# Kernel optimization log

Measured on AMD Instinct MI355X. Metric: run time of the kernel, lower is better.

## Reference

```python
import jax, jax.numpy as jnp
import numpy as np

B, S, T = 16, 256, 256
E, H = 1024, 512          # embedded_size = 2*hidden_size (required by the module's math)
ENV, ZHV = 32000, 32000


def gru_layer(x, h0, Wih, Whh, bih, bhh):
    # x: [B,T,in], h0: [B,H]; PyTorch GRU cell semantics
    xp = jnp.einsum('bti,gi->btg', x, Wih) + bih  # precompute input projections [B,T,3H]

    def step(h, xp_t):
        hp = h @ Whh.T + bhh
        xr, xz, xn = jnp.split(xp_t, 3, axis=-1)
        hr, hz, hn = jnp.split(hp, 3, axis=-1)
        r = jax.nn.sigmoid(xr + hr)
        z = jax.nn.sigmoid(xz + hz)
        n = jnp.tanh(xn + r * hn)
        h_new = (1.0 - z) * n + z * h
        return h_new, h_new

    h_last, ys = jax.lax.scan(step, h0, jnp.swapaxes(xp, 0, 1))
    return jnp.swapaxes(ys, 0, 1), h_last


def gru2(x, h0, p0, p1):
    # 2-layer stacked GRU; h0: [2,B,H]
    y0, h0f = gru_layer(x, h0[0], *p0)
    y1, h1f = gru_layer(y0, h0[1], *p1)
    return y1, jnp.stack([h0f, h1f])


def setup_inputs() -> dict:
    key = jax.random.key(0)
    ks = jax.random.split(key, 32)
    s = 0.05
    f = jnp.float32
    inp = {}
    inp['en_sen'] = jax.random.randint(ks[0], (B, S), 0, ENV)
    inp['zh_sen'] = jax.random.randint(ks[1], (B, T), 0, ZHV)
    inp['en_emb'] = (jax.random.normal(ks[2], (ENV, E)) * s).astype(f)
    inp['zh_emb'] = (jax.random.normal(ks[3], (ZHV, E)) * s).astype(f)
    inp['h0'] = jax.random.normal(ks[4], (2, B, H)).astype(f)
    i = 5
    for tag, in0 in (('e', E), ('d', E)):
        for layer, ind in ((0, in0), (1, H)):
            inp[f'Wih_{tag}{layer}'] = (jax.random.normal(ks[i], (3 * H, ind)) * s).astype(f); i += 1
            inp[f'Whh_{tag}{layer}'] = (jax.random.normal(ks[i], (3 * H, H)) * s).astype(f); i += 1
            inp[f'bih_{tag}{layer}'] = jnp.zeros((3 * H,), f)
            inp[f'bhh_{tag}{layer}'] = jnp.zeros((3 * H,), f)
    inp['fcW'] = (jax.random.normal(ks[i], (ZHV, E)) * s).astype(f)
    inp['fcb'] = jnp.zeros((ZHV,), f)
    return inp


def reference(en_sen, zh_sen, en_emb, zh_emb, h0,
              Wih_e0, Whh_e0, bih_e0, bhh_e0, Wih_e1, Whh_e1, bih_e1, bhh_e1,
              Wih_d0, Whh_d0, bih_d0, bhh_d0, Wih_d1, Whh_d1, bih_d1, bhh_d1,
              fcW, fcb):
    # encoder
    ex = en_emb[en_sen]                                     # [B,S,E]
    en_out, hid = gru2(ex, h0, (Wih_e0, Whh_e0, bih_e0, bhh_e0),
                       (Wih_e1, Whh_e1, bih_e1, bhh_e1))    # [B,S,H], [2,B,H]
    # shift target right with SOS token (zh_vocab_size - 2)
    sos = jnp.full((B, 1), ZHV - 2, dtype=zh_sen.dtype)
    zh = jnp.concatenate([sos, zh_sen[:, :-1]], axis=1)
    zx = zh_emb[zh]                                         # [B,T,E]
    # decoder (teacher forcing = 1.0 -> full-sequence scan is exact)
    dec_out, _ = gru2(zx, hid, (Wih_d0, Whh_d0, bih_d0, bhh_d0),
                      (Wih_d1, Whh_d1, bih_d1, bhh_d1))     # [B,T,H]
    # dot-product attention over encoder states, per decoder timestep
    scores = jnp.einsum('bsh,bth->bst', en_out, dec_out)    # [B,S,T]
    attn = jax.nn.softmax(scores, axis=1)                   # softmax over source dim
    ctx = jnp.einsum('bst,bsh->bth', attn, en_out)          # [B,T,H]
    de = jnp.concatenate([dec_out, ctx], axis=-1)           # [B,T,2H] == [B,T,E]
    out = de.reshape(-1, E) @ fcW.T + fcb                   # [B*T, ZHV]
    return out
```

## Files before the change

### kernel.cpp

```cpp
#include <hip/hip_runtime.h>
#include <math.h>

#define B_ 16
#define S_ 256
#define T_ 256
#define E_ 1024
#define H_ 512
#define G_ 1536
#define V_ 32000

typedef unsigned short u16;
typedef unsigned int u32;
typedef short short8 __attribute__((ext_vector_type(8)));
typedef short short4v __attribute__((ext_vector_type(4)));
typedef float f32x4 __attribute__((ext_vector_type(4)));

__device__ inline u16 f2bf(float x) {
  union { float f; unsigned u; } a; a.f = x;
  unsigned r = a.u + 0x7fff + ((a.u >> 16) & 1);
  return (u16)(r >> 16);
}
__device__ inline void split2(float x, u16& hi, u16& lo) {
  union { float f; unsigned u; } a; a.f = x;
  hi = (u16)(a.u >> 16);
  union { unsigned u; float f; } b; b.u = a.u & 0xffff0000u;
  lo = f2bf(x - b.f);
}

__device__ inline f32x4 load_f4_coh(const float* p) {
  f32x4 v;
  asm volatile("global_load_dwordx4 %0, %1, off sc0 sc1" : "=v"(v) : "v"(p));
  return v;
}

__device__ inline float dot4(f32x4 a, f32x4 b) {
  return a.x * b.x + a.y * b.y + a.z * b.z + a.w * b.w;
}

__global__ __launch_bounds__(256) void k_embed_enc(const int* __restrict__ sen,
                                                   const float* __restrict__ emb,
                                                   float* __restrict__ out) {
  long row = blockIdx.x;
  int tid = threadIdx.x;
  long e = sen[row];
  float4 v = *(const float4*)(emb + e * E_ + tid * 4);
  *(float4*)(out + row * E_ + tid * 4) = v;
}

__global__ __launch_bounds__(256) void k_embed_dec(const int* __restrict__ zh,
                                                   const float* __restrict__ emb,
                                                   float* __restrict__ out) {
  long row = blockIdx.x;
  int b = (int)(row >> 8), t = (int)(row & 255);
  int tid = threadIdx.x;
  long e = (t == 0) ? (V_ - 2) : zh[b * T_ + t - 1];
  float4 v = *(const float4*)(emb + e * E_ + tid * 4);
  *(float4*)(out + row * E_ + tid * 4) = v;
}

__global__ __launch_bounds__(256) void k_transpose(const float* __restrict__ in,
                                                   float* __restrict__ out, int R, int C) {
  __shared__ float tile[32][33];
  long z = blockIdx.z;
  const float* inz = in + z * (long)R * C;
  float* outz = out + z * (long)R * C;
  int x = blockIdx.x * 32 + threadIdx.x;
  int y0 = blockIdx.y * 32;
#pragma unroll
  for (int i = threadIdx.y; i < 32; i += 8)
    tile[i][threadIdx.x] = inz[(long)(y0 + i) * C + x];
  __syncthreads();
  int xo = y0 + threadIdx.x;
#pragma unroll
  for (int i = threadIdx.y; i < 32; i += 8) {
    int yo = blockIdx.x * 32 + i;
    outz[(long)yo * R + xo] = tile[threadIdx.x][i];
  }
}

__global__ __launch_bounds__(256) void k_gemm_nt(
    const float* __restrict__ A, int lda, const float* __restrict__ A2, int lda2, int kSplit,
    const float* __restrict__ Bm, int ldb, const float* __restrict__ bias,
    float* __restrict__ C, int ldc, int K, long sA, long sB, long sC) {
  __shared__ float As[8][132];
  __shared__ float Bs[8][132];
  int z = blockIdx.z;
  A += z * sA;
  Bm += z * sB;
  C += z * sC;
  int tid = threadIdx.x;
  int bm = blockIdx.y * 128, bn = blockIdx.x * 128;
  int tx = tid & 15, ty = tid >> 4;
  int lr = tid >> 1, lc = (tid & 1) * 4;
  float acc[8][8] = {};
  for (int k0 = 0; k0 < K; k0 += 8) {
    int ka = k0 + lc;
    const float* ap;
    if (A2 != nullptr && ka >= kSplit)
      ap = A2 + (long)(bm + lr) * lda2 + (ka - kSplit);
    else
      ap = A + (long)(bm + lr) * lda + ka;
    float4 a4 = *(const float4*)ap;
    float4 b4 = *(const float4*)(Bm + (long)(bn + lr) * ldb + k0 + lc);
    As[lc + 0][lr] = a4.x; As[lc + 1][lr] = a4.y; As[lc + 2][lr] = a4.z; As[lc + 3][lr] = a4.w;
    Bs[lc + 0][lr] = b4.x; Bs[lc + 1][lr] = b4.y; Bs[lc + 2][lr] = b4.z; Bs[lc + 3][lr] = b4.w;
    __syncthreads();
#pragma unroll
    for (int kk = 0; kk < 8; kk++) {
      float ar[8], br[8];
      *(float4*)&ar[0] = *(const float4*)&As[kk][ty * 8];
      *(float4*)&ar[4] = *(const float4*)&As[kk][ty * 8 + 4];
      *(float4*)&br[0] = *(const float4*)&Bs[kk][tx * 8];
      *(float4*)&br[4] = *(const float4*)&Bs[kk][tx * 8 + 4];
#pragma unroll
      for (int i = 0; i < 8; i++)
#pragma unroll
        for (int j = 0; j < 8; j++) acc[i][j] += ar[i] * br[j];
    }
    __syncthreads();
  }
  float bv[8];
#pragma unroll
  for (int j = 0; j < 8; j++) bv[j] = bias ? bias[bn + tx * 8 + j] : 0.f;
#pragma unroll
  for (int i = 0; i < 8; i++) {
    float* cp = C + (long)(bm + ty * 8 + i) * ldc + bn + tx * 8;
    float4 o0, o1;
    o0.x = acc[i][0] + bv[0]; o0.y = acc[i][1] + bv[1];
    o0.z = acc[i][2] + bv[2]; o0.w = acc[i][3] + bv[3];
    o1.x = acc[i][4] + bv[4]; o1.y = acc[i][5] + bv[5];
    o1.z = acc[i][6] + bv[6]; o1.w = acc[i][7] + bv[7];
    *(float4*)cp = o0;
    *(float4*)(cp + 4) = o1;
  }
}


__global__ __launch_bounds__(256) void k_gemm_mfma_nt(
    const float* __restrict__ A, int lda, const float* __restrict__ A2, int lda2, int kSplit,
    const float* __restrict__ Bm, int ldb, const float* __restrict__ bias,
    float* __restrict__ C, int ldc, int K) {
  __shared__ short8 Ah[512], Al[512], Bh[512], Bl[512];
  int tid = threadIdx.x;
  int bm = blockIdx.y * 128, bn = blockIdx.x * 128;
  int wave = tid >> 6, lane = tid & 63;
  int wm = (wave >> 1) * 64, wn = (wave & 1) * 64;
  int srow = tid >> 1, scol = (tid & 1) * 16, q0 = (tid & 1) * 2;
  int fr = lane & 15, fq = lane >> 4;
  int ubase = (srow >> 6) * 256 + ((srow >> 4) & 3) * 64;
  int ua0 = ubase + q0 * 16 + ((srow & 15) ^ (q0 * 2));
  int ua1 = ubase + (q0 + 1) * 16 + ((srow & 15) ^ (q0 * 2 + 2));
  int abase = (wm >> 6) * 256 + fq * 16 + (fr ^ (fq * 2));
  int bbase = (wn >> 6) * 256 + fq * 16 + (fr ^ (fq * 2));

  f32x4 acc[4][4] = {};

  for (int k0 = 0; k0 < K; k0 += 32) {
    {
      int ka = k0 + scol;
      const float* ap;
      if (A2 != nullptr && ka >= kSplit)
        ap = A2 + (long)(bm + srow) * lda2 + (ka - kSplit);
      else
        ap = A + (long)(bm + srow) * lda + ka;
      float va[16];
      *(float4*)&va[0] = *(const float4*)ap;
      *(float4*)&va[4] = *(const float4*)(ap + 4);
      *(float4*)&va[8] = *(const float4*)(ap + 8);
      *(float4*)&va[12] = *(const float4*)(ap + 12);
      u16 h[16], l[16];
#pragma unroll
      for (int i = 0; i < 16; i++) split2(va[i], h[i], l[i]);
      Ah[ua0] = *(short8*)&h[0];
      Ah[ua1] = *(short8*)&h[8];
      Al[ua0] = *(short8*)&l[0];
      Al[ua1] = *(short8*)&l[8];
    }
    {
      const float* bp = Bm + (long)(bn + srow) * ldb + k0 + scol;
      float vb[16];
      *(float4*)&vb[0] = *(const float4*)bp;
      *(float4*)&vb[4] = *(const float4*)(bp + 4);
      *(float4*)&vb[8] = *(const float4*)(bp + 8);
      *(float4*)&vb[12] = *(const float4*)(bp + 12);
      u16 h[16], l[16];
#pragma unroll
      for (int i = 0; i < 16; i++) split2(vb[i], h[i], l[i]);
      Bh[ua0] = *(short8*)&h[0];
      Bh[ua1] = *(short8*)&h[8];
      Bl[ua0] = *(short8*)&l[0];
      Bl[ua1] = *(short8*)&l[8];
    }
    __syncthreads();
    short8 afh[4], afl[4];
#pragma unroll
    for (int mt = 0; mt < 4; mt++) {
      afh[mt] = Ah[abase + mt * 64];
      afl[mt] = Al[abase + mt * 64];
    }
#pragma unroll
    for (int nt = 0; nt < 4; nt++) {
      short8 bh = Bh[bbase + nt * 64];
      short8 bl = Bl[bbase + nt * 64];
#pragma unroll
      for (int mt = 0; mt < 4; mt++) {
        acc[mt][nt] = __builtin_amdgcn_mfma_f32_16x16x32_bf16(afh[mt], bh, acc[mt][nt], 0, 0, 0);
        acc[mt][nt] = __builtin_amdgcn_mfma_f32_16x16x32_bf16(afh[mt], bl, acc[mt][nt], 0, 0, 0);
        acc[mt][nt] = __builtin_amdgcn_mfma_f32_16x16x32_bf16(afl[mt], bh, acc[mt][nt], 0, 0, 0);
      }
    }
    __syncthreads();
  }
  int fq4 = fq * 4;
#pragma unroll
  for (int nt = 0; nt < 4; nt++) {
    int col = bn + wn + nt * 16 + fr;
    float bv = bias ? bias[col] : 0.f;
#pragma unroll
    for (int mt = 0; mt < 4; mt++) {
      int row = bm + wm + mt * 16 + fq4;
#pragma unroll
      for (int j = 0; j < 4; j++)
        C[(long)(row + j) * ldc + col] = acc[mt][nt][j] + bv;
    }
  }
}

__global__ __launch_bounds__(256) void k_presplit(const float* __restrict__ src,
                                                  u16* __restrict__ hi,
                                                  u16* __restrict__ lo) {
  long i0 = ((long)blockIdx.x * 256 + threadIdx.x) * 8;
  float v[8];
  *(float4*)&v[0] = *(const float4*)(src + i0);
  *(float4*)&v[4] = *(const float4*)(src + i0 + 4);
  u16 h[8], l[8];
#pragma unroll
  for (int i = 0; i < 8; i++) split2(v[i], h[i], l[i]);
  *(short8*)(hi + i0) = *(short8*)&h[0];
  *(short8*)(lo + i0) = *(short8*)&l[0];
}

__global__ __launch_bounds__(256) void k_presplit_cat(const float* __restrict__ a,
                                                      const float* __restrict__ b,
                                                      u16* __restrict__ hi,
                                                      u16* __restrict__ lo) {
  long row = blockIdx.x;
  int tid = threadIdx.x;
  const float* src = (tid < 128) ? (a + row * 512 + tid * 4)
                                 : (b + row * 512 + (tid - 128) * 4);
  float4 v = *(const float4*)src;
  u16 h[4], l[4];
  split2(v.x, h[0], l[0]); split2(v.y, h[1], l[1]);
  split2(v.z, h[2], l[2]); split2(v.w, h[3], l[3]);
  *(short4v*)(hi + row * 1024 + tid * 4) = *(short4v*)&h[0];
  *(short4v*)(lo + row * 1024 + tid * 4) = *(short4v*)&l[0];
}

__global__ __launch_bounds__(256) void k_gemm_bf16p_nt(
    const u16* __restrict__ Ahi, const u16* __restrict__ Alo,
    const u16* __restrict__ Bhi, const u16* __restrict__ Blo,
    const float* __restrict__ bias, float* __restrict__ C, int ldc, int K) {
  __shared__ short8 Ah[512], Al[512], Bh[512], Bl[512];
  int tid = threadIdx.x;
  int bm = blockIdx.x * 128, bn = blockIdx.y * 128;
  int wave = tid >> 6, lane = tid & 63;
  int wm = (wave >> 1) * 64, wn = (wave & 1) * 64;
  int srow = tid >> 1, scol = (tid & 1) * 16, q0 = (tid & 1) * 2;
  int fr = lane & 15, fq = lane >> 4;
  int ubase = (srow >> 6) * 256 + ((srow >> 4) & 3) * 64;
  int ua0 = ubase + q0 * 16 + ((srow & 15) ^ (q0 * 2));
  int ua1 = ubase + (q0 + 1) * 16 + ((srow & 15) ^ (q0 * 2 + 2));
  int abase = (wm >> 6) * 256 + fq * 16 + (fr ^ (fq * 2));
  int bbase = (wn >> 6) * 256 + fq * 16 + (fr ^ (fq * 2));

  f32x4 acc[4][4] = {};
  long aoff = (long)(bm + srow) * K + scol;
  long boff = (long)(bn + srow) * K + scol;

  for (int k0 = 0; k0 < K; k0 += 32) {
    short8 ah0 = *(const short8*)(Ahi + aoff + k0);
    short8 ah1 = *(const short8*)(Ahi + aoff + k0 + 8);
    short8 al0 = *(const short8*)(Alo + aoff + k0);
    short8 al1 = *(const short8*)(Alo + aoff + k0 + 8);
    short8 bh0 = *(const short8*)(Bhi + boff + k0);
    short8 bh1 = *(const short8*)(Bhi + boff + k0 + 8);
    short8 bl0 = *(const short8*)(Blo + boff + k0);
    short8 bl1 = *(const short8*)(Blo + boff + k0 + 8);
    Ah[ua0] = ah0; Ah[ua1] = ah1;
    Al[ua0] = al0; Al[ua1] = al1;
    Bh[ua0] = bh0; Bh[ua1] = bh1;
    Bl[ua0] = bl0; Bl[ua1] = bl1;
    __syncthreads();
    short8 afh[4], afl[4];
#pragma unroll
    for (int mt = 0; mt < 4; mt++) {
      afh[mt] = Ah[abase + mt * 64];
      afl[mt] = Al[abase + mt * 64];
    }
#pragma unroll
    for (int nt = 0; nt < 4; nt++) {
      short8 bh = Bh[bbase + nt * 64];
      short8 bl = Bl[bbase + nt * 64];
#pragma unroll
      for (int mt = 0; mt < 4; mt++) {
        acc[mt][nt] = __builtin_amdgcn_mfma_f32_16x16x32_bf16(afh[mt], bh, acc[mt][nt], 0, 0, 0);
        acc[mt][nt] = __builtin_amdgcn_mfma_f32_16x16x32_bf16(afh[mt], bl, acc[mt][nt], 0, 0, 0);
        acc[mt][nt] = __builtin_amdgcn_mfma_f32_16x16x32_bf16(afl[mt], bh, acc[mt][nt], 0, 0, 0);
      }
    }
    __syncthreads();
  }
  int fq4 = fq * 4;
#pragma unroll
  for (int nt = 0; nt < 4; nt++) {
    int col = bn + wn + nt * 16 + fr;
    float bv = bias ? bias[col] : 0.f;
#pragma unroll
    for (int mt = 0; mt < 4; mt++) {
      int row = bm + wm + mt * 16 + fq4;
#pragma unroll
      for (int j = 0; j < 4; j++)
        C[(long)(row + j) * ldc + col] = acc[mt][nt][j] + bv;
    }
  }
}

#define WSLOT 32
__global__ __launch_bounds__(256) void k_gru_b(
    const float* __restrict__ xp, float* __restrict__ y,
    const float* __restrict__ Whh, const float* __restrict__ bhh,
    const float* __restrict__ hinit, long hbs, int* __restrict__ ep) {
  __shared__ float hls[536];
  int tid = threadIdx.x;
  int wave = tid >> 6, lane = tid & 63;
  int jsub = lane >> 5, ksl = lane & 31;
  int b = blockIdx.x >> 4, js = blockIdx.x & 15;
  int jbase = js * 32 + wave * 8 + jsub * 4;

  f32x4 w[4][3][4];
  float bb[4][3];
#pragma unroll
  for (int e = 0; e < 4; e++)
#pragma unroll
    for (int g = 0; g < 3; g++) {
      const float* r = Whh + (long)(g * 512 + jbase + e) * 512 + ksl * 16;
#pragma unroll
      for (int q = 0; q < 4; q++) w[e][g][q] = *(const f32x4*)(r + q * 4);
      bb[e][g] = bhh[g * 512 + jbase + e];
    }
  bool gl = (ksl < 4);
  int jme = jbase + ksl;
  const int* epb = ep + (long)(b * 16 + (lane & 15)) * WSLOT;
  int* epMine = ep + (long)(b * 16 + js) * WSLOT;
  float* yb = y + (long)b * (256 * 512);
  const float* xpb = xp + (long)b * (256 * 1536);

  for (int t = 0; t < 256; t++) {
    float xr = 0.f, xz = 0.f, xn = 0.f;
    if (gl) {
      const float* xpt = xpb + (long)t * 1536 + jme;
      xr = xpt[0]; xz = xpt[512]; xn = xpt[1024];
    }
    if (t > 0) {
      if (wave == 0) {
        while (true) {
          int e0;
          asm volatile("global_load_dword %0, %1, off sc0 sc1" : "=v"(e0) : "v"(epb));
          asm volatile("s_waitcnt vmcnt(0)" ::: "memory");
          if (__ballot(e0 >= t) == ~0ull) break;
          __builtin_amdgcn_s_sleep(1);
        }
      }
      __syncthreads();
    }
    if (tid < 128) {
      const float* src = (t == 0) ? (hinit + (long)b * hbs + tid * 4)
                                  : (yb + (long)(t - 1) * 512 + tid * 4);
      f32x4 v = load_f4_coh(src);
      asm volatile("s_waitcnt vmcnt(0)" ::: "memory");
      __builtin_amdgcn_sched_barrier(0);
      *(f32x4*)&hls[(tid & 3) * 132 + (tid >> 2) * 4] = v;
    }
    __syncthreads();
    f32x4 h0 = *(const f32x4*)&hls[ksl * 4];
    f32x4 h1 = *(const f32x4*)&hls[132 + ksl * 4];
    f32x4 h2 = *(const f32x4*)&hls[264 + ksl * 4];
    f32x4 h3 = *(const f32x4*)&hls[396 + ksl * 4];
    float a[4][3];
#pragma unroll
    for (int e = 0; e < 4; e++)
#pragma unroll
      for (int g = 0; g < 3; g++)
        a[e][g] = dot4(h0, w[e][g][0]) + dot4(h1, w[e][g][1]) +
                  dot4(h2, w[e][g][2]) + dot4(h3, w[e][g][3]);
#pragma unroll
    for (int m = 1; m <= 16; m <<= 1)
#pragma unroll
      for (int e = 0; e < 4; e++) {
        a[e][0] += __shfl_xor(a[e][0], m);
        a[e][1] += __shfl_xor(a[e][1], m);
        a[e][2] += __shfl_xor(a[e][2], m);
      }
    if (gl) {
      float hr = 0.f, hz = 0.f, hn = 0.f, Br = 0.f, Bz = 0.f, Bn = 0.f;
#pragma unroll
      for (int e = 0; e < 4; e++)
        if (ksl == e) {
          hr = a[e][0]; hz = a[e][1]; hn = a[e][2];
          Br = bb[e][0]; Bz = bb[e][1]; Bn = bb[e][2];
        }
      float r = 1.f / (1.f + __expf(-(xr + hr + Br)));
      float z = 1.f / (1.f + __expf(-(xz + hz + Bz)));
      float n = tanhf(xn + r * (hn + Bn));
      float hp = hls[((jme >> 2) & 3) * 132 + (jme >> 4) * 4 + (jme & 3)];
      float hv = (1.f - z) * n + z * hp;
      __hip_atomic_store(&yb[(long)t * 512 + jme], hv,
                         __ATOMIC_RELAXED, __HIP_MEMORY_SCOPE_AGENT);
    }
    asm volatile("s_waitcnt vmcnt(0)" ::: "memory");
    __syncthreads();
    if (tid == 0)
      __hip_atomic_store(epMine, t + 1, __ATOMIC_RELAXED, __HIP_MEMORY_SCOPE_AGENT);
  }
}

__global__ __launch_bounds__(256) void k_softmax(float* __restrict__ p) {
  long row = blockIdx.x;
  int tid = threadIdx.x;
  float* pr = p + row * 256;
  float v = pr[tid];
  float m = v;
#pragma unroll
  for (int off = 32; off >= 1; off >>= 1) m = fmaxf(m, __shfl_xor(m, off));
  __shared__ float wmax[4];
  __shared__ float wsum[4];
  int wv = tid >> 6, ln = tid & 63;
  if (ln == 0) wmax[wv] = m;
  __syncthreads();
  m = fmaxf(fmaxf(wmax[0], wmax[1]), fmaxf(wmax[2], wmax[3]));
  float e = expf(v - m);
  float s = e;
#pragma unroll
  for (int off = 32; off >= 1; off >>= 1) s += __shfl_xor(s, off);
  if (ln == 0) wsum[wv] = s;
  __syncthreads();
  s = wsum[0] + wsum[1] + wsum[2] + wsum[3];
  pr[tid] = e / s;
}

extern "C" void kernel_launch(void* const* d_in, const int* in_sizes, int n_in,
                              void* d_out, int out_size, void* d_ws, size_t ws_size,
                              hipStream_t stream) {
  const int* en_sen = (const int*)d_in[0];
  const int* zh_sen = (const int*)d_in[1];
  const float* en_emb = (const float*)d_in[2];
  const float* zh_emb = (const float*)d_in[3];
  const float* h0 = (const float*)d_in[4];
  const float* Wih_e0 = (const float*)d_in[5];
  const float* Whh_e0 = (const float*)d_in[6];
  const float* bih_e0 = (const float*)d_in[7];
  const float* bhh_e0 = (const float*)d_in[8];
  const float* Wih_e1 = (const float*)d_in[9];
  const float* Whh_e1 = (const float*)d_in[10];
  const float* bih_e1 = (const float*)d_in[11];
  const float* bhh_e1 = (const float*)d_in[12];
  const float* Wih_d0 = (const float*)d_in[13];
  const float* Whh_d0 = (const float*)d_in[14];
  const float* bih_d0 = (const float*)d_in[15];
  const float* bhh_d0 = (const float*)d_in[16];
  const float* Wih_d1 = (const float*)d_in[17];
  const float* Whh_d1 = (const float*)d_in[18];
  const float* bih_d1 = (const float*)d_in[19];
  const float* bhh_d1 = (const float*)d_in[20];
  const float* fcW = (const float*)d_in[21];
  const float* fcb = (const float*)d_in[22];
  float* out = (float*)d_out;

  const size_t needFast = (2ull * 32768000 + 2ull * 4194304) * sizeof(u16);
  bool fastFC = (ws_size >= needFast);

  u16* fcWhi = (u16*)d_ws;
  u16* fcWlo = fcWhi + 32768000;
  u16* Ahi = (u16*)(fcWlo + 32768000);
  u16* Alo = Ahi + 4194304;

  int* flags = (int*)d_out;
  float* bufE = (float*)d_out + 32768;
  float* xp = bufE + 4194304;
  float* bufY = xp + 6291456;
  float* enOut = bufY + 2097152;
  float* scT = enOut + 2097152;
  float* enOutT = scT + 1048576;
  float* decOutA = enOutT + 2097152;
  float* ctxA = decOutA + 2097152;

  float* decOut = fastFC ? decOutA : (float*)d_ws;
  float* ctx = fastFC ? ctxA : ((float*)d_ws + 2097152);

  hipMemsetAsync(flags, 0, 32768 * sizeof(int), stream);

  dim3 tb(32, 8);

  if (fastFC)
    k_presplit<<<16000, 256, 0, stream>>>(fcW, fcWhi, fcWlo);

  k_embed_enc<<<B_ * S_, 256, 0, stream>>>(en_sen, en_emb, bufE);
  k_gemm_mfma_nt<<<dim3(G_ / 128, (B_ * S_) / 128, 1), 256, 0, stream>>>(
      bufE, E_, nullptr, 0, E_, Wih_e0, E_, bih_e0, xp, G_, E_);
  k_gru_b<<<256, 256, 0, stream>>>(xp, bufY, Whh_e0, bhh_e0, h0, (long)H_, flags);
  k_gemm_mfma_nt<<<dim3(G_ / 128, (B_ * S_) / 128, 1), 256, 0, stream>>>(
      bufY, H_, nullptr, 0, H_, Wih_e1, H_, bih_e1, xp, G_, H_);
  k_gru_b<<<256, 256, 0, stream>>>(xp, enOut, Whh_e1, bhh_e1, h0 + B_ * H_, (long)H_,
                                   flags + 8192);

  k_embed_dec<<<B_ * T_, 256, 0, stream>>>(zh_sen, zh_emb, bufE);
  k_gemm_mfma_nt<<<dim3(G_ / 128, (B_ * T_) / 128, 1), 256, 0, stream>>>(
      bufE, E_, nullptr, 0, E_, Wih_d0, E_, bih_d0, xp, G_, E_);
  k_gru_b<<<256, 256, 0, stream>>>(xp, bufY, Whh_d0, bhh_d0, bufY + 255 * H_,
                                   (long)(256 * H_), flags + 16384);
  k_gemm_mfma_nt<<<dim3(G_ / 128, (B_ * T_) / 128, 1), 256, 0, stream>>>(
      bufY, H_, nullptr, 0, H_, Wih_d1, H_, bih_d1, xp, G_, H_);
  k_gru_b<<<256, 256, 0, stream>>>(xp, decOut, Whh_d1, bhh_d1, enOut + 255 * H_,
                                   (long)(256 * H_), flags + 24576);

  k_gemm_nt<<<dim3(S_ / 128, T_ / 128, B_), 256, 0, stream>>>(
      decOut, H_, nullptr, 0, H_, enOut, H_, nullptr, scT, S_, H_,
      (long)T_ * H_, (long)S_ * H_, (long)T_ * S_);
  k_softmax<<<B_ * T_, 256, 0, stream>>>(scT);
  k_transpose<<<dim3(16, 8, B_), tb, 0, stream>>>(enOut, enOutT, 256, 512);
  k_gemm_nt<<<dim3(H_ / 128, T_ / 128, B_), 256, 0, stream>>>(
      scT, S_, nullptr, 0, S_, enOutT, S_, nullptr, ctx, H_, S_,
      (long)T_ * S_, (long)H_ * S_, (long)T_ * H_);

  if (fastFC) {
    k_presplit_cat<<<B_ * T_, 256, 0, stream>>>(decOut, ctx, Ahi, Alo);
    k_gemm_bf16p_nt<<<dim3((B_ * T_) / 128, V_ / 128, 1), 256, 0, stream>>>(
        Ahi, Alo, fcWhi, fcWlo, fcb, out, V_, E_);
  } else {
    k_gemm_mfma_nt<<<dim3(V_ / 128, (B_ * T_) / 128, 1), 256, 0, stream>>>(
        decOut, H_, ctx, H_, H_, fcW, E_, fcb, out, V_, E_);
  }
}
```

Measured before the change: 4.593 ms.

## Replace per-block epoch flags with value-plus-tag packets in GRU recurrence

The cross-block synchronisation in the persistent GRU kernel changes from per-block epoch flags to packets that pair each hidden value with its timestep tag. Each thread now polls two packets directly and writes them into shared memory, so the separate flag spin, the barrier, the coherent h reload and the store-drain before publishing the flag all go away. In exchange the sync buffer grows to 64 MB, which adds a larger memset and more coherent traffic per step, and every thread spins on global memory instead of a single wave.

```diff
diff --git a/kernel.cpp b/kernel.cpp
--- a/kernel.cpp
+++ b/kernel.cpp
@@ -14,6 +14,7 @@
 typedef short short8 __attribute__((ext_vector_type(8)));
 typedef short short4v __attribute__((ext_vector_type(4)));
 typedef float f32x4 __attribute__((ext_vector_type(4)));
+typedef unsigned int u32x2 __attribute__((ext_vector_type(2)));
 
 __device__ inline u16 f2bf(float x) {
   union { float f; unsigned u; } a; a.f = x;
@@ -325,11 +326,10 @@
   }
 }
 
-#define WSLOT 32
 __global__ __launch_bounds__(256) void k_gru_b(
     const float* __restrict__ xp, float* __restrict__ y,
     const float* __restrict__ Whh, const float* __restrict__ bhh,
-    const float* __restrict__ hinit, long hbs, int* __restrict__ ep) {
+    const float* __restrict__ hinit, long hbs, u32* __restrict__ pkt) {
   __shared__ float hls[536];
   int tid = threadIdx.x;
   int wave = tid >> 6, lane = tid & 63;
@@ -350,10 +350,12 @@
     }
   bool gl = (ksl < 4);
   int jme = jbase + ksl;
-  const int* epb = ep + (long)(b * 16 + (lane & 15)) * WSLOT;
-  int* epMine = ep + (long)(b * 16 + js) * WSLOT;
   float* yb = y + (long)b * (256 * 512);
   const float* xpb = xp + (long)b * (256 * 1536);
+  u32* pkb = pkt + (long)b * (256 * 512 * 2);
+  int cj0 = tid, cj1 = tid + 256;
+  int cp0 = ((cj0 >> 2) & 3) * 132 + (cj0 >> 4) * 4 + (cj0 & 3);
+  int cp1 = ((cj1 >> 2) & 3) * 132 + (cj1 >> 4) * 4 + (cj1 & 3);
 
   for (int t = 0; t < 256; t++) {
     float xr = 0.f, xz = 0.f, xn = 0.f;
@@ -362,20 +364,22 @@
       xr = xpt[0]; xz = xpt[512]; xn = xpt[1024];
     }
     if (t > 0) {
-      if (wave == 0) {
-        while (true) {
-          int e0;
-          asm volatile("global_load_dword %0, %1, off sc0 sc1" : "=v"(e0) : "v"(epb));
-          asm volatile("s_waitcnt vmcnt(0)" ::: "memory");
-          if (__ballot(e0 >= t) == ~0ull) break;
-          __builtin_amdgcn_s_sleep(1);
-        }
+      const u32* pp0 = pkb + ((long)(t - 1) * 512 + cj0) * 2;
+      const u32* pp1 = pkb + ((long)(t - 1) * 512 + cj1) * 2;
+      u32x2 p0, p1;
+      while (true) {
+        asm volatile("global_load_dwordx2 %0, %1, off sc0 sc1" : "=v"(p0) : "v"(pp0));
+        asm volatile("global_load_dwordx2 %0, %1, off sc0 sc1" : "=v"(p1) : "v"(pp1));
+        asm volatile("s_waitcnt vmcnt(0)" ::: "memory");
+        if (p0.y == (u32)t && p1.y == (u32)t) break;
+        __builtin_amdgcn_s_sleep(1);
       }
-      __syncthreads();
-    }
-    if (tid < 128) {
-      const float* src = (t == 0) ? (hinit + (long)b * hbs + tid * 4)
-                                  : (yb + (long)(t - 1) * 512 + tid * 4);
+      union { u32 u; float f; } c0, c1;
+      c0.u = p0.x; c1.u = p1.x;
+      hls[cp0] = c0.f;
+      hls[cp1] = c1.f;
+    } else if (tid < 128) {
+      const float* src = hinit + (long)b * hbs + tid * 4;
       f32x4 v = load_f4_coh(src);
       asm volatile("s_waitcnt vmcnt(0)" ::: "memory");
       __builtin_amdgcn_sched_barrier(0);
@@ -414,13 +418,14 @@
       float n = tanhf(xn + r * (hn + Bn));
       float hp = hls[((jme >> 2) & 3) * 132 + (jme >> 4) * 4 + (jme & 3)];
       float hv = (1.f - z) * n + z * hp;
-      __hip_atomic_store(&yb[(long)t * 512 + jme], hv,
-                         __ATOMIC_RELAXED, __HIP_MEMORY_SCOPE_AGENT);
-    }
-    asm volatile("s_waitcnt vmcnt(0)" ::: "memory");
-    __syncthreads();
-    if (tid == 0)
-      __hip_atomic_store(epMine, t + 1, __ATOMIC_RELAXED, __HIP_MEMORY_SCOPE_AGENT);
+      union { float f; u32 u; } hb; hb.f = hv;
+      u32x2 pkv;
+      pkv.x = hb.u; pkv.y = (u32)(t + 1);
+      asm volatile("global_store_dwordx2 %0, %1, off sc0 sc1"
+                   ::"v"(pkb + ((long)t * 512 + jme) * 2), "v"(pkv) : "memory");
+      yb[(long)t * 512 + jme] = hv;
+    }
+    __syncthreads();
   }
 }
 
@@ -484,8 +489,9 @@
   u16* Ahi = (u16*)(fcWlo + 32768000);
   u16* Alo = Ahi + 4194304;
 
-  int* flags = (int*)d_out;
-  float* bufE = (float*)d_out + 32768;
+  const long PKL = 4194304;
+  u32* pkts = (u32*)d_out;
+  float* bufE = (float*)d_out + 16777216;
   float* xp = bufE + 4194304;
   float* bufY = xp + 6291456;
   float* enOut = bufY + 2097152;
@@ -497,7 +503,7 @@
   float* decOut = fastFC ? decOutA : (float*)d_ws;
   float* ctx = fastFC ? ctxA : ((float*)d_ws + 2097152);
 
-  hipMemsetAsync(flags, 0, 32768 * sizeof(int), stream);
+  hipMemsetAsync(pkts, 0, 4 * PKL * sizeof(u32), stream);
 
   dim3 tb(32, 8);
 
@@ -507,21 +513,21 @@
   k_embed_enc<<<B_ * S_, 256, 0, stream>>>(en_sen, en_emb, bufE);
   k_gemm_mfma_nt<<<dim3(G_ / 128, (B_ * S_) / 128, 1), 256, 0, stream>>>(
       bufE, E_, nullptr, 0, E_, Wih_e0, E_, bih_e0, xp, G_, E_);
-  k_gru_b<<<256, 256, 0, stream>>>(xp, bufY, Whh_e0, bhh_e0, h0, (long)H_, flags);
+  k_gru_b<<<256, 256, 0, stream>>>(xp, bufY, Whh_e0, bhh_e0, h0, (long)H_, pkts);
   k_gemm_mfma_nt<<<dim3(G_ / 128, (B_ * S_) / 128, 1), 256, 0, stream>>>(
       bufY, H_, nullptr, 0, H_, Wih_e1, H_, bih_e1, xp, G_, H_);
   k_gru_b<<<256, 256, 0, stream>>>(xp, enOut, Whh_e1, bhh_e1, h0 + B_ * H_, (long)H_,
-                                   flags + 8192);
+                                   pkts + PKL);
 
   k_embed_dec<<<B_ * T_, 256, 0, stream>>>(zh_sen, zh_emb, bufE);
   k_gemm_mfma_nt<<<dim3(G_ / 128, (B_ * T_) / 128, 1), 256, 0, stream>>>(
       bufE, E_, nullptr, 0, E_, Wih_d0, E_, bih_d0, xp, G_, E_);
   k_gru_b<<<256, 256, 0, stream>>>(xp, bufY, Whh_d0, bhh_d0, bufY + 255 * H_,
-                                   (long)(256 * H_), flags + 16384);
+                                   (long)(256 * H_), pkts + 2 * PKL);
   k_gemm_mfma_nt<<<dim3(G_ / 128, (B_ * T_) / 128, 1), 256, 0, stream>>>(
       bufY, H_, nullptr, 0, H_, Wih_d1, H_, bih_d1, xp, G_, H_);
   k_gru_b<<<256, 256, 0, stream>>>(xp, decOut, Whh_d1, bhh_d1, enOut + 255 * H_,
-                                   (long)(256 * H_), flags + 24576);
+                                   (long)(256 * H_), pkts + 3 * PKL);
 
   k_gemm_nt<<<dim3(S_ / 128, T_ / 128, B_), 256, 0, stream>>>(
       decOut, H_, nullptr, 0, H_, enOut, H_, nullptr, scT, S_, H_,
```

Result: faster. 3.998 ms (-13.0%).
